# Kernel optimization log

Hardware: AMD Instinct MI355X
Metric: run time of the kernel (lower is better)

Reference implementation:

```python
import jax, jax.numpy as jnp
import numpy as np

N_NODES = 100000
N_EDGES = 600000
N_FEAT = 128
HIDDEN = 128
N_CLASSES = 40  # output dim = num_classes + 1 = 41


def setup_inputs() -> dict:
    key = jax.random.key(0)
    k = jax.random.split(key, 6)
    x = jax.random.normal(k[0], (N_NODES, N_FEAT), dtype=jnp.float32)
    edge_index = jax.random.randint(k[1], (2, N_EDGES), 0, N_NODES, dtype=jnp.int64)
    # GCNConv params (Glorot-ish scale)
    W1 = jax.random.normal(k[2], (N_FEAT, HIDDEN), dtype=jnp.float32) / np.sqrt(N_FEAT)
    b1 = jnp.zeros((HIDDEN,), dtype=jnp.float32)
    W2 = jax.random.normal(k[3], (HIDDEN, N_CLASSES + 1), dtype=jnp.float32) / np.sqrt(HIDDEN)
    b2 = jnp.zeros((N_CLASSES + 1,), dtype=jnp.float32)
    return {"x": x, "W1": W1, "b1": b1, "W2": W2, "b2": b2, "edge_index": edge_index}


def _gcn_layer(x, W, b, src, dst, norm, n):
    # linear transform then normalized scatter-add aggregation (PyG GCNConv)
    h = x @ W                                  # [N, out]
    msg = h[src] * norm[:, None]               # gather + per-edge normalization
    out = jax.ops.segment_sum(msg, dst, num_segments=n)
    return out + b


def reference(x, W1, b1, W2, b2, edge_index):
    n = x.shape[0]
    # add self-loops
    loops = jnp.arange(n, dtype=edge_index.dtype)
    src = jnp.concatenate([edge_index[0], loops])
    dst = jnp.concatenate([edge_index[1], loops])
    # symmetric degree normalization: D^{-1/2} A_hat D^{-1/2}
    deg = jax.ops.segment_sum(jnp.ones_like(dst, dtype=x.dtype), dst, num_segments=n)
    dinv = jnp.where(deg > 0, jax.lax.rsqrt(deg), 0.0)
    norm = dinv[src] * dinv[dst]               # [E + N]
    h = _gcn_layer(x, W1, b1, src, dst, norm, n)
    h = jax.nn.relu(h)
    # dropout is identity in eval mode
    h = _gcn_layer(h, W2, b2, src, dst, norm, n)
    return jax.nn.log_softmax(h, axis=1)
```

## Files before the change

kernel.cpp:

```cpp
#include <hip/hip_runtime.h>
#include <math.h>

#define N_NODES 100000
#define N_EDGES 600000
#define NC 41
#define NB ((N_NODES + 255) / 256)
#define PREB 2048
#define CNTB ((N_EDGES + 255) / 256)

typedef __attribute__((ext_vector_type(8))) short bf16x8;
typedef __attribute__((ext_vector_type(8))) unsigned short u16x8;
typedef __attribute__((ext_vector_type(4))) float f32x4;

static __device__ __forceinline__ unsigned short f2b(float f) {
    unsigned u = __float_as_uint(f);
    unsigned r = ((u >> 16) & 1u) + 0x7fffu;
    return (unsigned short)((u + r) >> 16);
}
static __device__ __forceinline__ float b2f(unsigned short s) {
    return __uint_as_float(((unsigned)s) << 16);
}
static __device__ __forceinline__ u16x8 zero8() {
    u16x8 z;
#pragma unroll
    for (int i = 0; i < 8; ++i) z[i] = 0;
    return z;
}

__global__ __launch_bounds__(256) void k_prep(const float* __restrict__ x,
                                              unsigned short* __restrict__ xb,
                                              const int* __restrict__ dst,
                                              int* __restrict__ cnt) {
    int tid = blockIdx.x * 256 + threadIdx.x;
    const int nthr = PREB * 256;
    for (int i = tid; i < N_NODES * 128 / 8; i += nthr) {
        float4 lo = ((const float4*)x)[i * 2];
        float4 hi = ((const float4*)x)[i * 2 + 1];
        u16x8 o;
        o[0] = f2b(lo.x); o[1] = f2b(lo.y); o[2] = f2b(lo.z); o[3] = f2b(lo.w);
        o[4] = f2b(hi.x); o[5] = f2b(hi.y); o[6] = f2b(hi.z); o[7] = f2b(hi.w);
        ((u16x8*)xb)[i] = o;
    }
    for (int e = tid; e < N_EDGES; e += nthr)
        atomicAdd(&cnt[dst[e]], 1);
}

__global__ __launch_bounds__(256) void k_blocksum(const int* __restrict__ cnt,
                                                  int* __restrict__ bsum,
                                                  float* __restrict__ dinv, int n) {
    __shared__ int tmp[256];
    int t = threadIdx.x, gid = blockIdx.x * 256 + t;
    int v = (gid < n) ? cnt[gid] : 0;
    if (gid < n) dinv[gid] = rsqrtf((float)(v + 1));
    tmp[t] = v;
    __syncthreads();
    for (int d = 128; d; d >>= 1) {
        if (t < d) tmp[t] += tmp[t + d];
        __syncthreads();
    }
    if (t == 0) bsum[blockIdx.x] = tmp[0];
}

__global__ __launch_bounds__(512) void k_scanb(int* __restrict__ bsum, int nb) {
    __shared__ int tmp[512];
    int t = threadIdx.x;
    int v = (t < nb) ? bsum[t] : 0;
    tmp[t] = v;
    __syncthreads();
    for (int d = 1; d < 512; d <<= 1) {
        int u = (t >= d) ? tmp[t - d] : 0;
        __syncthreads();
        tmp[t] += u;
        __syncthreads();
    }
    if (t < nb) bsum[t] = tmp[t] - v;
}

__global__ __launch_bounds__(256) void k_scanfinal(int* __restrict__ cnt,
                                                   const int* __restrict__ bsum,
                                                   int* __restrict__ off, int n) {
    __shared__ int tmp[256];
    int t = threadIdx.x, gid = blockIdx.x * 256 + t;
    int v = (gid < n) ? cnt[gid] : 0;
    tmp[t] = v;
    __syncthreads();
    for (int d = 1; d < 256; d <<= 1) {
        int u = (t >= d) ? tmp[t - d] : 0;
        __syncthreads();
        tmp[t] += u;
        __syncthreads();
    }
    int ex = tmp[t] - v + bsum[blockIdx.x];
    if (gid < n) {
        off[gid] = ex;
        cnt[gid] = ex;
    }
    if (gid == 0) off[n] = N_EDGES;
}

__global__ void k_scatter(const int* __restrict__ src, const int* __restrict__ dst,
                          const float* __restrict__ dinv,
                          int* __restrict__ cursor, int2* __restrict__ eidx, int E) {
    int e = blockIdx.x * blockDim.x + threadIdx.x;
    if (e >= E) return;
    int s = src[e];
    int d = dst[e];
    float ds = dinv[s];
    int pos = atomicAdd(&cursor[d], 1);
    eidx[pos] = make_int2(s, __float_as_int(ds));
}

__global__ __launch_bounds__(256, 8) void k_aggx(const unsigned short* __restrict__ xb,
                                                 const float* __restrict__ dinv,
                                                 const int* __restrict__ off,
                                                 const int2* __restrict__ eidx,
                                                 unsigned short* __restrict__ R) {
    int tid = threadIdx.x;
    int node = blockIdx.x * 16 + (tid >> 4);
    int j = tid & 15;
    float di = dinv[node];
    float acc[8];
    {
        u16x8 v = *(const u16x8*)(xb + (size_t)node * 128 + j * 8);
#pragma unroll
        for (int i = 0; i < 8; ++i) acc[i] = b2f(v[i]) * di;
    }
    int beg = off[node], end = off[node + 1];
    int e = beg;
    int2 p0 = (e < end) ? eidx[e] : make_int2(-1, 0);
    int2 p1 = (e + 1 < end) ? eidx[e + 1] : make_int2(-1, 0);
    u16x8 r0 = zero8(), r1 = zero8();
    if (p0.x >= 0) r0 = *(const u16x8*)(xb + (size_t)p0.x * 128 + j * 8);
    if (p1.x >= 0) r1 = *(const u16x8*)(xb + (size_t)p1.x * 128 + j * 8);
    while (p0.x >= 0) {
        int2 p2 = (e + 2 < end) ? eidx[e + 2] : make_int2(-1, 0);
        u16x8 r2 = zero8();
        if (p2.x >= 0) r2 = *(const u16x8*)(xb + (size_t)p2.x * 128 + j * 8);
        float nm = __int_as_float(p0.y);
#pragma unroll
        for (int i = 0; i < 8; ++i) acc[i] = fmaf(b2f(r0[i]), nm, acc[i]);
        p0 = p1; p1 = p2; r0 = r1; r1 = r2; ++e;
    }
    u16x8 o;
#pragma unroll
    for (int i = 0; i < 8; ++i) o[i] = f2b(acc[i] * di);
    *(u16x8*)(R + (size_t)node * 128 + j * 8) = o;
}

__global__ __launch_bounds__(512) void k_mm(const unsigned short* __restrict__ R,
                                            const float* __restrict__ W1,
                                            const float* __restrict__ b1,
                                            const float* __restrict__ W2,
                                            const float* __restrict__ dinv,
                                            unsigned short* __restrict__ h2) {
    __shared__ unsigned short Wt1[128 * 132];
    __shared__ unsigned short Wt2[48 * 132];
    __shared__ unsigned short rows[32 * 136];
    int tid = threadIdx.x;
    for (int i = tid; i < 128 * 128; i += 512) {
        int k = i >> 7, n = i & 127;
        Wt1[n * 132 + k] = f2b(W1[i]);
    }
    for (int i = tid; i < 128 * 48; i += 512) {
        int k = i / 48, n = i % 48;
        Wt2[n * 132 + k] = f2b((n < NC) ? W2[k * NC + n] : 0.f);
    }
    __syncthreads();

    int l = tid & 63, w = tid >> 6;
    int lr = l & 15, g = l >> 4;
    int rh = w >> 2;
    int cg = w & 3;
    int rh2 = w / 3, ct = w % 3;

    bf16x8 f1[2][4];
#pragma unroll
    for (int c = 0; c < 2; ++c) {
        int n = (cg * 2 + c) * 16 + lr;
#pragma unroll
        for (int kt = 0; kt < 4; ++kt) {
            const unsigned short* p = &Wt1[n * 132 + kt * 32 + g * 4];
            short4 lo = *(const short4*)p;
            short4 hi = *(const short4*)(p + 16);
            bf16x8 f;
            f[0] = lo.x; f[1] = lo.y; f[2] = lo.z; f[3] = lo.w;
            f[4] = hi.x; f[5] = hi.y; f[6] = hi.z; f[7] = hi.w;
            f1[c][kt] = f;
        }
    }
    bf16x8 f2[4];
    if (w < 6) {
#pragma unroll
        for (int kt = 0; kt < 4; ++kt) {
            const unsigned short* p = &Wt2[(ct * 16 + lr) * 132 + kt * 32 + g * 4];
            short4 lo = *(const short4*)p;
            short4 hi = *(const short4*)(p + 16);
            bf16x8 f;
            f[0] = lo.x; f[1] = lo.y; f[2] = lo.z; f[3] = lo.w;
            f[4] = hi.x; f[5] = hi.y; f[6] = hi.z; f[7] = hi.w;
            f2[kt] = f;
        }
    }
    float bia0 = b1[(cg * 2) * 16 + lr];
    float bia1 = b1[(cg * 2 + 1) * 16 + lr];

    int srow = tid >> 4, scol = tid & 15;
    for (int t = blockIdx.x; t < N_NODES / 32; t += gridDim.x) {
        *(u16x8*)&rows[srow * 136 + scol * 8] =
            *(const u16x8*)(R + ((size_t)t * 32 + srow) * 128 + scol * 8);
        __syncthreads();

        f32x4 a0 = {0.f, 0.f, 0.f, 0.f};
        f32x4 a1 = {0.f, 0.f, 0.f, 0.f};
#pragma unroll
        for (int kt = 0; kt < 4; ++kt) {
            const unsigned short* pa = &rows[(rh * 16 + lr) * 136 + kt * 32 + g * 4];
            short4 alo = *(const short4*)pa;
            short4 ahi = *(const short4*)(pa + 16);
            bf16x8 a;
            a[0] = alo.x; a[1] = alo.y; a[2] = alo.z; a[3] = alo.w;
            a[4] = ahi.x; a[5] = ahi.y; a[6] = ahi.z; a[7] = ahi.w;
            a0 = __builtin_amdgcn_mfma_f32_16x16x32_bf16(a, f1[0][kt], a0, 0, 0, 0);
            a1 = __builtin_amdgcn_mfma_f32_16x16x32_bf16(a, f1[1][kt], a1, 0, 0, 0);
        }
        __syncthreads();

#pragma unroll
        for (int i = 0; i < 4; ++i) {
            int row = rh * 16 + g * 4 + i;
            rows[row * 136 + (cg * 2) * 16 + lr]     = f2b(fmaxf(a0[i] + bia0, 0.f));
            rows[row * 136 + (cg * 2 + 1) * 16 + lr] = f2b(fmaxf(a1[i] + bia1, 0.f));
        }
        __syncthreads();

        if (w < 6) {
            f32x4 c0 = {0.f, 0.f, 0.f, 0.f};
#pragma unroll
            for (int kt = 0; kt < 4; ++kt) {
                const unsigned short* pa = &rows[(rh2 * 16 + lr) * 136 + kt * 32 + g * 4];
                short4 alo = *(const short4*)pa;
                short4 ahi = *(const short4*)(pa + 16);
                bf16x8 a;
                a[0] = alo.x; a[1] = alo.y; a[2] = alo.z; a[3] = alo.w;
                a[4] = ahi.x; a[5] = ahi.y; a[6] = ahi.z; a[7] = ahi.w;
                c0 = __builtin_amdgcn_mfma_f32_16x16x32_bf16(a, f2[kt], c0, 0, 0, 0);
            }
#pragma unroll
            for (int i = 0; i < 4; ++i) {
                int row = t * 32 + rh2 * 16 + g * 4 + i;
                h2[(size_t)row * 64 + ct * 16 + lr] = f2b(c0[i] * dinv[row]);
            }
        }
        __syncthreads();
    }
}

__global__ __launch_bounds__(256, 8) void k_gather2(const unsigned short* __restrict__ h2,
                                                    float* __restrict__ out,
                                                    const int* __restrict__ off,
                                                    const int2* __restrict__ eidx,
                                                    const float* __restrict__ dinv,
                                                    const float* __restrict__ b2) {
    __shared__ float so[8 * NC + 8];
    int tid = threadIdx.x;
    int nloc = tid >> 5;
    int node = blockIdx.x * 8 + nloc;
    int l = tid & 31;
    int g = l >> 3, j = l & 7;
    bool act = (j < 6);
    float di = dinv[node];
    float acc[8];
#pragma unroll
    for (int i = 0; i < 8; ++i) acc[i] = 0.f;
    if (g == 0 && act) {
        u16x8 v = *(const u16x8*)(h2 + (size_t)node * 64 + j * 8);
#pragma unroll
        for (int i = 0; i < 8; ++i) acc[i] = b2f(v[i]);
    }
    int beg = off[node], end = off[node + 1];
    int e = beg + g;
    int s0 = (e < end) ? eidx[e].x : -1;
    int s1 = (e + 4 < end) ? eidx[e + 4].x : -1;
    u16x8 r0 = zero8(), r1 = zero8();
    if (s0 >= 0 && act) r0 = *(const u16x8*)(h2 + (size_t)s0 * 64 + j * 8);
    if (s1 >= 0 && act) r1 = *(const u16x8*)(h2 + (size_t)s1 * 64 + j * 8);
    while (s0 >= 0) {
        int s2 = (e + 8 < end) ? eidx[e + 8].x : -1;
        u16x8 r2 = zero8();
        if (s2 >= 0 && act) r2 = *(const u16x8*)(h2 + (size_t)s2 * 64 + j * 8);
#pragma unroll
        for (int i = 0; i < 8; ++i) acc[i] += b2f(r0[i]);
        s0 = s1; s1 = s2; r0 = r1; r1 = r2; e += 4;
    }
#pragma unroll
    for (int i = 0; i < 8; ++i) acc[i] += __shfl_xor(acc[i], 8);
#pragma unroll
    for (int i = 0; i < 8; ++i) acc[i] += __shfl_xor(acc[i], 16);
    int c0 = j * 8;
    float vv[8];
#pragma unroll
    for (int i = 0; i < 8; ++i)
        vv[i] = (act && c0 + i < NC) ? acc[i] * di + b2[c0 + i] : -INFINITY;
    float m = vv[0];
#pragma unroll
    for (int i = 1; i < 8; ++i) m = fmaxf(m, vv[i]);
#pragma unroll
    for (int o = 4; o; o >>= 1) m = fmaxf(m, __shfl_xor(m, o));
    float sm = 0.f;
#pragma unroll
    for (int i = 0; i < 8; ++i) sm += (act && c0 + i < NC) ? expf(vv[i] - m) : 0.f;
#pragma unroll
    for (int o = 4; o; o >>= 1) sm += __shfl_xor(sm, o);
    float lg = logf(sm);
    if (g == 0 && act) {
#pragma unroll
        for (int i = 0; i < 8; ++i) {
            int c = c0 + i;
            if (c < NC) so[nloc * NC + c] = vv[i] - m - lg;
        }
    }
    __syncthreads();
    float4* ob = (float4*)(out + (size_t)blockIdx.x * (8 * NC));
    const float4* sb = (const float4*)so;
    if (tid < 2 * NC) ob[tid] = sb[tid];
}

extern "C" void kernel_launch(void* const* d_in, const int* in_sizes, int n_in,
                              void* d_out, int out_size, void* d_ws, size_t ws_size,
                              hipStream_t stream) {
    const float* x  = (const float*)d_in[0];
    const float* W1 = (const float*)d_in[1];
    const float* b1 = (const float*)d_in[2];
    const float* W2 = (const float*)d_in[3];
    const float* b2 = (const float*)d_in[4];
    const int*   ei = (const int*)d_in[5];
    const int* src = ei;
    const int* dst = ei + N_EDGES;
    float* out = (float*)d_out;

    char* ws = (char*)d_ws;
    int*   cnt  = (int*)ws;
    int*   off  = cnt + N_NODES + 32;
    int*   bsum = off + N_NODES + 32;
    float* dinv = (float*)(bsum + 512);
    int2*  eidx = (int2*)(dinv + N_NODES + 32);
    unsigned short* xb = (unsigned short*)(ws + (8u << 20));
    unsigned short* R  = xb + (size_t)N_NODES * 128;
    unsigned short* h2 = R + (size_t)N_NODES * 128;

    hipMemsetAsync(cnt, 0, N_NODES * sizeof(int), stream);
    k_prep<<<PREB, 256, 0, stream>>>(x, xb, dst, cnt);
    k_blocksum<<<NB, 256, 0, stream>>>(cnt, bsum, dinv, N_NODES);
    k_scanb<<<1, 512, 0, stream>>>(bsum, NB);
    k_scanfinal<<<NB, 256, 0, stream>>>(cnt, bsum, off, N_NODES);
    k_scatter<<<CNTB, 256, 0, stream>>>(src, dst, dinv, cnt, eidx, N_EDGES);

    k_aggx<<<N_NODES / 16, 256, 0, stream>>>(xb, dinv, off, eidx, R);
    k_mm<<<1024, 512, 0, stream>>>(R, W1, b1, W2, dinv, h2);

    k_gather2<<<N_NODES / 8, 256, 0, stream>>>(h2, out, off, eidx, dinv, b2);
}
```

Baseline: 186.6 us.

## Pre-scale bf16 features by dinv and shrink CSR edge entries to int

The bf16 conversion of x now happens after the degree scan, so each row is pre-multiplied by its dinv value. The layer-1 aggregation then reduces to plain adds, and the CSR entries drop from int2 (src, dinv) to a single int. Edge counting moves into its own small kernel, and the fp32-to-bf16 conversion is fused with the edge scatter. This halves the edge-index traffic and removes per-edge multiplies, at the cost of the conversion now waiting on the scan, which loses the earlier overlap of conversion with counting.

```diff
diff --git a/kernel.cpp b/kernel.cpp
--- a/kernel.cpp
+++ b/kernel.cpp
@@ -5,7 +5,7 @@
 #define N_EDGES 600000
 #define NC 41
 #define NB ((N_NODES + 255) / 256)
-#define PREB 2048
+#define BLDB 2048
 #define CNTB ((N_EDGES + 255) / 256)
 
 typedef __attribute__((ext_vector_type(8))) short bf16x8;
@@ -27,22 +27,9 @@
     return z;
 }
 
-__global__ __launch_bounds__(256) void k_prep(const float* __restrict__ x,
-                                              unsigned short* __restrict__ xb,
-                                              const int* __restrict__ dst,
-                                              int* __restrict__ cnt) {
-    int tid = blockIdx.x * 256 + threadIdx.x;
-    const int nthr = PREB * 256;
-    for (int i = tid; i < N_NODES * 128 / 8; i += nthr) {
-        float4 lo = ((const float4*)x)[i * 2];
-        float4 hi = ((const float4*)x)[i * 2 + 1];
-        u16x8 o;
-        o[0] = f2b(lo.x); o[1] = f2b(lo.y); o[2] = f2b(lo.z); o[3] = f2b(lo.w);
-        o[4] = f2b(hi.x); o[5] = f2b(hi.y); o[6] = f2b(hi.z); o[7] = f2b(hi.w);
-        ((u16x8*)xb)[i] = o;
-    }
-    for (int e = tid; e < N_EDGES; e += nthr)
-        atomicAdd(&cnt[dst[e]], 1);
+__global__ void k_count(const int* __restrict__ dst, int* __restrict__ cnt, int E) {
+    int e = blockIdx.x * blockDim.x + threadIdx.x;
+    if (e < E) atomicAdd(&cnt[dst[e]], 1);
 }
 
 __global__ __launch_bounds__(256) void k_blocksum(const int* __restrict__ cnt,
@@ -98,22 +85,38 @@
     if (gid == 0) off[n] = N_EDGES;
 }
 
-__global__ void k_scatter(const int* __restrict__ src, const int* __restrict__ dst,
-                          const float* __restrict__ dinv,
-                          int* __restrict__ cursor, int2* __restrict__ eidx, int E) {
-    int e = blockIdx.x * blockDim.x + threadIdx.x;
-    if (e >= E) return;
-    int s = src[e];
-    int d = dst[e];
-    float ds = dinv[s];
-    int pos = atomicAdd(&cursor[d], 1);
-    eidx[pos] = make_int2(s, __float_as_int(ds));
+__global__ __launch_bounds__(256) void k_build(const float* __restrict__ x,
+                                               const float* __restrict__ dinv,
+                                               unsigned short* __restrict__ xb,
+                                               const int* __restrict__ src,
+                                               const int* __restrict__ dst,
+                                               int* __restrict__ cursor,
+                                               int* __restrict__ eidx) {
+    int tid = blockIdx.x * 256 + threadIdx.x;
+    const int nthr = BLDB * 256;
+    for (int i = tid; i < N_NODES * 16; i += nthr) {
+        float di = dinv[i >> 4];
+        float4 lo = ((const float4*)x)[i * 2];
+        float4 hi = ((const float4*)x)[i * 2 + 1];
+        u16x8 o;
+        o[0] = f2b(lo.x * di); o[1] = f2b(lo.y * di);
+        o[2] = f2b(lo.z * di); o[3] = f2b(lo.w * di);
+        o[4] = f2b(hi.x * di); o[5] = f2b(hi.y * di);
+        o[6] = f2b(hi.z * di); o[7] = f2b(hi.w * di);
+        ((u16x8*)xb)[i] = o;
+    }
+    for (int e = tid; e < N_EDGES; e += nthr) {
+        int s = src[e];
+        int d = dst[e];
+        int pos = atomicAdd(&cursor[d], 1);
+        eidx[pos] = s;
+    }
 }
 
 __global__ __launch_bounds__(256, 8) void k_aggx(const unsigned short* __restrict__ xb,
                                                  const float* __restrict__ dinv,
                                                  const int* __restrict__ off,
-                                                 const int2* __restrict__ eidx,
+                                                 const int* __restrict__ eidx,
                                                  unsigned short* __restrict__ R) {
     int tid = threadIdx.x;
     int node = blockIdx.x * 16 + (tid >> 4);
@@ -123,23 +126,22 @@
     {
         u16x8 v = *(const u16x8*)(xb + (size_t)node * 128 + j * 8);
 #pragma unroll
-        for (int i = 0; i < 8; ++i) acc[i] = b2f(v[i]) * di;
+        for (int i = 0; i < 8; ++i) acc[i] = b2f(v[i]);
     }
     int beg = off[node], end = off[node + 1];
     int e = beg;
-    int2 p0 = (e < end) ? eidx[e] : make_int2(-1, 0);
-    int2 p1 = (e + 1 < end) ? eidx[e + 1] : make_int2(-1, 0);
+    int s0 = (e < end) ? eidx[e] : -1;
+    int s1 = (e + 1 < end) ? eidx[e + 1] : -1;
     u16x8 r0 = zero8(), r1 = zero8();
-    if (p0.x >= 0) r0 = *(const u16x8*)(xb + (size_t)p0.x * 128 + j * 8);
-    if (p1.x >= 0) r1 = *(const u16x8*)(xb + (size_t)p1.x * 128 + j * 8);
-    while (p0.x >= 0) {
-        int2 p2 = (e + 2 < end) ? eidx[e + 2] : make_int2(-1, 0);
+    if (s0 >= 0) r0 = *(const u16x8*)(xb + (size_t)s0 * 128 + j * 8);
+    if (s1 >= 0) r1 = *(const u16x8*)(xb + (size_t)s1 * 128 + j * 8);
+    while (s0 >= 0) {
+        int s2 = (e + 2 < end) ? eidx[e + 2] : -1;
         u16x8 r2 = zero8();
-        if (p2.x >= 0) r2 = *(const u16x8*)(xb + (size_t)p2.x * 128 + j * 8);
-        float nm = __int_as_float(p0.y);
-#pragma unroll
-        for (int i = 0; i < 8; ++i) acc[i] = fmaf(b2f(r0[i]), nm, acc[i]);
-        p0 = p1; p1 = p2; r0 = r1; r1 = r2; ++e;
+        if (s2 >= 0) r2 = *(const u16x8*)(xb + (size_t)s2 * 128 + j * 8);
+#pragma unroll
+        for (int i = 0; i < 8; ++i) acc[i] += b2f(r0[i]);
+        s0 = s1; s1 = s2; r0 = r1; r1 = r2; ++e;
     }
     u16x8 o;
 #pragma unroll
@@ -258,7 +260,7 @@
 __global__ __launch_bounds__(256, 8) void k_gather2(const unsigned short* __restrict__ h2,
                                                     float* __restrict__ out,
                                                     const int* __restrict__ off,
-                                                    const int2* __restrict__ eidx,
+                                                    const int* __restrict__ eidx,
                                                     const float* __restrict__ dinv,
                                                     const float* __restrict__ b2) {
     __shared__ float so[8 * NC + 8];
@@ -279,13 +281,13 @@
     }
     int beg = off[node], end = off[node + 1];
     int e = beg + g;
-    int s0 = (e < end) ? eidx[e].x : -1;
-    int s1 = (e + 4 < end) ? eidx[e + 4].x : -1;
+    int s0 = (e < end) ? eidx[e] : -1;
+    int s1 = (e + 4 < end) ? eidx[e + 4] : -1;
     u16x8 r0 = zero8(), r1 = zero8();
     if (s0 >= 0 && act) r0 = *(const u16x8*)(h2 + (size_t)s0 * 64 + j * 8);
     if (s1 >= 0 && act) r1 = *(const u16x8*)(h2 + (size_t)s1 * 64 + j * 8);
     while (s0 >= 0) {
-        int s2 = (e + 8 < end) ? eidx[e + 8].x : -1;
+        int s2 = (e + 8 < end) ? eidx[e + 8] : -1;
         u16x8 r2 = zero8();
         if (s2 >= 0 && act) r2 = *(const u16x8*)(h2 + (size_t)s2 * 64 + j * 8);
 #pragma unroll
@@ -343,17 +345,18 @@
     int*   off  = cnt + N_NODES + 32;
     int*   bsum = off + N_NODES + 32;
     float* dinv = (float*)(bsum + 512);
-    int2*  eidx = (int2*)(dinv + N_NODES + 32);
+    int*   eidx = (int*)(dinv + N_NODES + 32);
     unsigned short* xb = (unsigned short*)(ws + (8u << 20));
     unsigned short* R  = xb + (size_t)N_NODES * 128;
     unsigned short* h2 = R + (size_t)N_NODES * 128;
 
     hipMemsetAsync(cnt, 0, N_NODES * sizeof(int), stream);
-    k_prep<<<PREB, 256, 0, stream>>>(x, xb, dst, cnt);
+    k_count<<<CNTB, 256, 0, stream>>>(dst, cnt, N_EDGES);
     k_blocksum<<<NB, 256, 0, stream>>>(cnt, bsum, dinv, N_NODES);
     k_scanb<<<1, 512, 0, stream>>>(bsum, NB);
     k_scanfinal<<<NB, 256, 0, stream>>>(cnt, bsum, off, N_NODES);
-    k_scatter<<<CNTB, 256, 0, stream>>>(src, dst, dinv, cnt, eidx, N_EDGES);
+
+    k_build<<<BLDB, 256, 0, stream>>>(x, dinv, xb, src, dst, cnt, eidx);
 
     k_aggx<<<N_NODES / 16, 256, 0, stream>>>(xb, dinv, off, eidx, R);
     k_mm<<<1024, 512, 0, stream>>>(R, W1, b1, W2, dinv, h2);
```

Result: no change. 183.4 us (-1.7%).
